# Performance work log

Measured on AMD Instinct MI355X. Metric: run time of the kernel, lower is better.

Reference implementation:

```python
import jax, jax.numpy as jnp
import numpy as np

N = 100_000      # nodes
E = 3_200_000    # directed edges (avg degree 32)
F_IN = 5         # node_features
H = 64           # hidden_dim


def setup_inputs() -> dict:
    key = jax.random.key(0)
    ks = jax.random.split(key, 11)
    x = jax.random.uniform(ks[0], (N, F_IN), dtype=jnp.float32)
    edge_index = jax.random.randint(ks[1], (2, E), 0, N, dtype=jnp.int32)
    def lin(k, fi, fo):
        kw, kb = jax.random.split(k)
        s = 1.0 / np.sqrt(fi)
        return (jax.random.uniform(kw, (fi, fo), jnp.float32, -s, s),
                jax.random.uniform(kb, (fo,), jnp.float32, -s, s))
    conv1_w, conv1_b = lin(ks[2], F_IN, H)
    conv2_w, conv2_b = lin(ks[3], H, H)
    lin1_w, lin1_b = lin(ks[4], H + 6, 32)
    lin2_w, lin2_b = lin(ks[5], 32, 2)
    return {"x": x, "edge_index": edge_index,
            "conv1_w": conv1_w, "conv1_b": conv1_b,
            "conv2_w": conv2_w, "conv2_b": conv2_b,
            "lin1_w": lin1_w, "lin1_b": lin1_b,
            "lin2_w": lin2_w, "lin2_b": lin2_b}


def _gcn_conv(x, src, dst, norm, W, b):
    # PyG GCNConv: out[dst] += norm_e * (x @ W)[src], then + bias
    h = x @ W                                   # [N, out]
    msg = h[src] * norm[:, None]                # [E+N, out] (gather, memory-bound)
    out = jax.ops.segment_sum(msg, dst, num_segments=N)
    return out + b


def _global_features(x):
    n_comp = jnp.sum(x[:, 2])
    n_and = jnp.sum(x[:, 3])
    n_or = jnp.sum(x[:, 4])
    comp_mask = (x[:, 2] == 1.0).astype(x.dtype)
    cnt = jnp.sum(comp_mask)
    safe = jnp.maximum(cnt, 1.0)
    avg_lambda = jnp.where(cnt > 0, jnp.sum(x[:, 0] * comp_mask) / safe, 0.0)
    avg_mu = jnp.where(cnt > 0, jnp.sum(x[:, 1] * comp_mask) / safe, 0.0)
    depth = n_and + n_or
    gf = jnp.stack([n_comp, n_and, n_or, depth, avg_lambda, avg_mu])[None, :]
    # original uses .item() -> constants, so no grad flows through these
    return jax.lax.stop_gradient(gf)


def reference(x, edge_index, conv1_w, conv1_b, conv2_w, conv2_b,
              lin1_w, lin1_b, lin2_w, lin2_b):
    loop = jnp.arange(N, dtype=edge_index.dtype)
    src = jnp.concatenate([edge_index[0], loop])   # add self-loops
    dst = jnp.concatenate([edge_index[1], loop])
    deg = jax.ops.segment_sum(jnp.ones_like(src, dtype=x.dtype), dst, num_segments=N)
    dinv = jnp.where(deg > 0, 1.0 / jnp.sqrt(deg), 0.0)
    norm = dinv[src] * dinv[dst]                   # [E+N]

    h = jax.nn.relu(_gcn_conv(x, src, dst, norm, conv1_w, conv1_b))
    h = jax.nn.relu(_gcn_conv(h, src, dst, norm, conv2_w, conv2_b))

    # global_mean_pool with batch == zeros -> mean over all nodes, one graph
    emb = jnp.mean(h, axis=0, keepdims=True)       # [1, H]
    emb = jnp.concatenate([emb, _global_features(x)], axis=1)  # [1, H+6]

    hid = jax.nn.relu(emb @ lin1_w + lin1_b)
    raw = hid @ lin2_w + lin2_b                    # [1, 2]
    return 2.0 + jax.nn.sigmoid(raw) * 3.0
```

## Files before the change

### kernel.cpp

```cpp
#include <hip/hip_runtime.h>
#include <hip/hip_bf16.h>
#include <math.h>


#define BUCKET 256
#define MAXB   512
#define NCHV   2048
#define Q      8
#define RCOPY  32

__global__ void k_hist(const int* __restrict__ dst, int E, int chunk,
                       int* __restrict__ gcounts, int NBK) {
    __shared__ int lcnt[MAXB];
    for (int i = threadIdx.x; i < NBK; i += blockDim.x) lcnt[i] = 0;
    __syncthreads();
    int e0 = blockIdx.x * chunk;
    int e1 = min(e0 + chunk, E);
    for (int e = e0 + threadIdx.x; e < e1; e += blockDim.x)
        atomicAdd(&lcnt[dst[e] >> 8], 1);
    __syncthreads();
    for (int b = threadIdx.x; b < NBK; b += blockDim.x)
        gcounts[blockIdx.x * NBK + b] = lcnt[b];
}

__global__ void k_colsum(const int* __restrict__ gcounts, int* __restrict__ btot,
                         int NBK, int NCH) {
    __shared__ int lds[256];
    int b = blockIdx.x, t = threadIdx.x;
    int s = 0;
    for (int c = t; c < NCH; c += 256) s += gcounts[c * NBK + b];
    lds[t] = s;
    __syncthreads();
    for (int off = 128; off; off >>= 1) {
        if (t < off) lds[t] += lds[t + off];
        __syncthreads();
    }
    if (t == 0) btot[b] = lds[0];
}

__global__ void k_scanA(const int* __restrict__ btot, int* __restrict__ bucket_base,
                        float* __restrict__ red, int NBK) {
    __shared__ int lds[MAXB];
    int t = threadIdx.x;
    for (int i = t; i < RCOPY * 64; i += MAXB) red[i] = 0.f;
    int v = (t < NBK) ? btot[t] : 0;
    lds[t] = v;
    __syncthreads();
    for (int off = 1; off < MAXB; off <<= 1) {
        int add = (t >= off) ? lds[t - off] : 0;
        __syncthreads();
        lds[t] += add;
        __syncthreads();
    }
    if (t < NBK) bucket_base[t] = lds[t] - v;
    if (t == NBK - 1) bucket_base[NBK] = lds[t];
}

__global__ void k_scanB(int* __restrict__ gcounts, const int* __restrict__ bucket_base,
                        int NBK, int NCH) {
    __shared__ int lds[512];
    int b = blockIdx.x, t = threadIdx.x;
    int carry = bucket_base[b];
    for (int base = 0; base < NCH; base += 512) {
        int c = base + t;
        int v = (c < NCH) ? gcounts[c * NBK + b] : 0;
        lds[t] = v;
        __syncthreads();
        for (int off = 1; off < 512; off <<= 1) {
            int add = (t >= off) ? lds[t - off] : 0;
            __syncthreads();
            lds[t] += add;
            __syncthreads();
        }
        if (c < NCH) gcounts[c * NBK + b] = carry + lds[t] - v;
        int tot = lds[511];
        __syncthreads();
        carry += tot;
    }
}

__global__ void k_bucketize(const int* __restrict__ src, const int* __restrict__ dst,
                            int E, int chunk, const int* __restrict__ gcounts,
                            int* __restrict__ records, int NBK) {
    __shared__ int lcur[MAXB];
    for (int b = threadIdx.x; b < NBK; b += blockDim.x)
        lcur[b] = gcounts[blockIdx.x * NBK + b];
    __syncthreads();
    int e0 = blockIdx.x * chunk;
    int e1 = min(e0 + chunk, E);
    for (int e = e0 + threadIdx.x; e < e1; e += blockDim.x) {
        int d = dst[e];
        int b = d >> 8;
        int rec = ((d & 255) << 17) | src[e];
        int slot = atomicAdd(&lcur[b], 1);
        records[slot] = rec;
    }
}

__global__ void k_csrA(const int* __restrict__ records, const int* __restrict__ bucket_base,
                       int* __restrict__ qhist) {
    __shared__ int cnt[BUCKET];
    int t = threadIdx.x, b = blockIdx.x, q = blockIdx.y;
    if (t < BUCKET) cnt[t] = 0;
    __syncthreads();
    int j0 = bucket_base[b], j1 = bucket_base[b + 1];
    int qlen = (j1 - j0 + Q - 1) / Q;
    int qs = j0 + q * qlen;
    int qe = min(qs + qlen, j1);
    for (int j = qs + t; j < qe; j += blockDim.x)
        atomicAdd(&cnt[records[j] >> 17], 1);
    __syncthreads();
    if (t < BUCKET) qhist[(b * Q + q) * BUCKET + t] = cnt[t];
}

__global__ void k_csrB(const int* __restrict__ qhist, const int* __restrict__ bucket_base,
                       const float* __restrict__ x,
                       int* __restrict__ qbase, int* __restrict__ pos,
                       int* __restrict__ rowend, float* __restrict__ dinv,
                       float* __restrict__ xs, float* __restrict__ gfpart, int n) {
    __shared__ int lds[BUCKET];
    __shared__ float gf6[8];
    int t = threadIdx.x, b = blockIdx.x;
    if (t < 8) gf6[t] = 0.f;
    int h[Q];
    int c = 0;
#pragma unroll
    for (int q = 0; q < Q; ++q) {
        h[q] = qhist[(b * Q + q) * BUCKET + t];
        c += h[q];
    }
    lds[t] = c;
    __syncthreads();
    for (int off = 1; off < BUCKET; off <<= 1) {
        int add = (t >= off) ? lds[t - off] : 0;
        __syncthreads();
        lds[t] += add;
        __syncthreads();
    }
    int j0 = bucket_base[b];
    int p = j0 + lds[t] - c;
    int run = p;
#pragma unroll
    for (int q = 0; q < Q; ++q) {
        qbase[(b * Q + q) * BUCKET + t] = run;
        run += h[q];
    }
    int node = b * BUCKET + t;
    float s2 = 0.f, s3 = 0.f, s4 = 0.f, sm0 = 0.f, sm1 = 0.f, sc = 0.f;
    if (node < n) {
        pos[node] = p;
        rowend[node] = p + c;
        float d = rsqrtf((float)(c + 1));
        dinv[node] = d;
        float x0 = x[node * 5 + 0], x1 = x[node * 5 + 1], x2 = x[node * 5 + 2];
        float x3 = x[node * 5 + 3], x4 = x[node * 5 + 4];
        float4 o;
        o.x = x0 * d; o.y = x1 * d; o.z = x2 * d; o.w = x3 * d;
        ((float4*)xs)[node * 2] = o;
        xs[node * 8 + 4] = x4 * d;
        s2 = x2; s3 = x3; s4 = x4;
        if (x2 == 1.0f) { sm0 = x0; sm1 = x1; sc = 1.f; }
    }
#pragma unroll
    for (int off = 32; off; off >>= 1) {
        s2 += __shfl_down(s2, off);
        s3 += __shfl_down(s3, off);
        s4 += __shfl_down(s4, off);
        sm0 += __shfl_down(sm0, off);
        sm1 += __shfl_down(sm1, off);
        sc += __shfl_down(sc, off);
    }
    if ((t & 63) == 0) {
        atomicAdd(&gf6[0], s2);
        atomicAdd(&gf6[1], s3);
        atomicAdd(&gf6[2], s4);
        atomicAdd(&gf6[3], sm0);
        atomicAdd(&gf6[4], sm1);
        atomicAdd(&gf6[5], sc);
    }
    __syncthreads();
    if (t < 6) gfpart[b * 8 + t] = gf6[t];
}

__global__ void k_csrC(const int* __restrict__ records, const int* __restrict__ bucket_base,
                       const int* __restrict__ qbase, int* __restrict__ ssrc) {
    __shared__ int cursor[BUCKET];
    int t = threadIdx.x, b = blockIdx.x, q = blockIdx.y;
    if (t < BUCKET) cursor[t] = qbase[(b * Q + q) * BUCKET + t];
    __syncthreads();
    int j0 = bucket_base[b], j1 = bucket_base[b + 1];
    int qlen = (j1 - j0 + Q - 1) / Q;
    int qs = j0 + q * qlen;
    int qe = min(qs + qlen, j1);
    for (int j = qs + t; j < qe; j += blockDim.x) {
        int rec = records[j];
        int slot = atomicAdd(&cursor[rec >> 17], 1);
        ssrc[slot] = rec & 131071;
    }
}

__global__ void k_agg5(const int* __restrict__ pos, const int* __restrict__ rowend,
                       const int* __restrict__ ssrc, const float* __restrict__ dinv,
                       const float* __restrict__ xs, float* __restrict__ agg5, int n) {
    int i = blockIdx.x * blockDim.x + threadIdx.x;
    if (i >= n) return;
    const float4* xs4 = (const float4*)xs;
    float4 a = xs4[i * 2];
    float a4 = xs[i * 8 + 4];
    int beg = pos[i], end = rowend[i];
    int j = beg;
    for (; j + 1 < end; j += 2) {
        int s0 = ssrc[j], s1 = ssrc[j + 1];
        float4 v0 = xs4[s0 * 2]; float w0 = xs[s0 * 8 + 4];
        float4 v1 = xs4[s1 * 2]; float w1 = xs[s1 * 8 + 4];
        a.x += v0.x + v1.x; a.y += v0.y + v1.y;
        a.z += v0.z + v1.z; a.w += v0.w + v1.w;
        a4 += w0 + w1;
    }
    for (; j < end; ++j) {
        int s = ssrc[j];
        float4 v = xs4[s * 2];
        a.x += v.x; a.y += v.y; a.z += v.z; a.w += v.w;
        a4 += xs[s * 8 + 4];
    }
    float dd = dinv[i];
    float4 o; o.x = a.x * dd; o.y = a.y * dd; o.z = a.z * dd; o.w = a.w * dd;
    ((float4*)agg5)[i * 2] = o;
    agg5[i * 8 + 4] = a4 * dd;
}

__global__ void k_h1(const float* __restrict__ agg5, const float* __restrict__ W1,
                     const float* __restrict__ b1, const float* __restrict__ dinv,
                     __hip_bfloat16* __restrict__ h1s, int n) {
    int t = blockIdx.x * blockDim.x + threadIdx.x;
    int i = t >> 6, f = t & 63;
    if (i >= n) return;
    float a0 = agg5[i * 8 + 0], a1 = agg5[i * 8 + 1], a2 = agg5[i * 8 + 2];
    float a3 = agg5[i * 8 + 3], a4 = agg5[i * 8 + 4];
    float v = a0 * W1[f] + a1 * W1[64 + f] + a2 * W1[128 + f]
            + a3 * W1[192 + f] + a4 * W1[256 + f] + b1[f];
    h1s[(size_t)i * 64 + f] = __float2bfloat16(dinv[i] * fmaxf(v, 0.f));
}

__global__ __launch_bounds__(256)
void k_l2fuse(const int* __restrict__ pos, const int* __restrict__ rowend,
              const int* __restrict__ ssrc, const float* __restrict__ dinv,
              const __hip_bfloat16* __restrict__ h1s, const float* __restrict__ W2,
              const float* __restrict__ b2, float* __restrict__ red, int n) {
    __shared__ float red64[64];
    int t = threadIdx.x, f = t & 63;
    if (t < 64) red64[t] = 0.f;
    __syncthreads();
    int w = blockIdx.x * (blockDim.x >> 6) + (t >> 6);
    int nw = gridDim.x * (blockDim.x >> 6);
    float bf = b2[f];
    float psum = 0.f;
    int nt = (n + 3) >> 2;
    for (int task = w; task < nt; task += nw) {
        int i0 = task * 4, i1 = i0 + 1, i2 = i0 + 2, i3 = i0 + 3;
        bool v1 = i1 < n, v2 = i2 < n, v3 = i3 < n;
        int p0 = pos[i0],            e0 = rowend[i0];
        int p1 = v1 ? pos[i1] : 0,   e1 = v1 ? rowend[i1] : 0;
        int p2 = v2 ? pos[i2] : 0,   e2 = v2 ? rowend[i2] : 0;
        int p3 = v3 ? pos[i3] : 0,   e3 = v3 ? rowend[i3] : 0;
        float a0 = __bfloat162float(h1s[(size_t)i0 * 64 + f]);
        float a1 = v1 ? __bfloat162float(h1s[(size_t)i1 * 64 + f]) : 0.f;
        float a2 = v2 ? __bfloat162float(h1s[(size_t)i2 * 64 + f]) : 0.f;
        float a3 = v3 ? __bfloat162float(h1s[(size_t)i3 * 64 + f]) : 0.f;
        int len = max(max(e0 - p0, e1 - p1), max(e2 - p2, e3 - p3));
#pragma unroll 2
        for (int m = 0; m < len; ++m) {
            int j0 = p0 + m, j1 = p1 + m, j2 = p2 + m, j3 = p3 + m;
            int s0 = ssrc[j0 < e0 ? j0 : 0];
            int s1 = ssrc[j1 < e1 ? j1 : 0];
            int s2 = ssrc[j2 < e2 ? j2 : 0];
            int s3 = ssrc[j3 < e3 ? j3 : 0];
            float g0 = __bfloat162float(h1s[(size_t)s0 * 64 + f]);
            float g1 = __bfloat162float(h1s[(size_t)s1 * 64 + f]);
            float g2 = __bfloat162float(h1s[(size_t)s2 * 64 + f]);
            float g3 = __bfloat162float(h1s[(size_t)s3 * 64 + f]);
            if (j0 < e0) a0 += g0;
            if (j1 < e1) a1 += g1;
            if (j2 < e2) a2 += g2;
            if (j3 < e3) a3 += g3;
        }
        float q0 = 0.f, q1 = 0.f, q2 = 0.f, q3 = 0.f;
#pragma unroll 8
        for (int k = 0; k < 64; ++k) {
            float w2v = W2[k * 64 + f];
            q0 += __shfl(a0, k) * w2v;
            q1 += __shfl(a1, k) * w2v;
            q2 += __shfl(a2, k) * w2v;
            q3 += __shfl(a3, k) * w2v;
        }
        psum += fmaxf(q0 * dinv[i0] + bf, 0.f);
        if (v1) psum += fmaxf(q1 * dinv[i1] + bf, 0.f);
        if (v2) psum += fmaxf(q2 * dinv[i2] + bf, 0.f);
        if (v3) psum += fmaxf(q3 * dinv[i3] + bf, 0.f);
    }
    atomicAdd(&red64[f], psum);
    __syncthreads();
    if (t < 64) atomicAdd(&red[(blockIdx.x & (RCOPY - 1)) * 64 + t], red64[t]);
}

__global__ void k_head(const float* __restrict__ red, const float* __restrict__ gfpart,
                       const float* __restrict__ l1w, const float* __restrict__ l1b,
                       const float* __restrict__ l2w, const float* __restrict__ l2b,
                       float* __restrict__ out, int n, int NBK) {
    __shared__ float emb[70];
    __shared__ float hid[32];
    int t = threadIdx.x;
    if (t < 64) {
        float s = 0.f;
#pragma unroll
        for (int c = 0; c < RCOPY; ++c) s += red[c * 64 + t];
        emb[t] = s / (float)n;
    }
    float g0 = 0.f, g1 = 0.f, g2 = 0.f, g3 = 0.f, g4 = 0.f, g5 = 0.f;
    for (int b = t; b < NBK; b += 64) {
        g0 += gfpart[b * 8 + 0]; g1 += gfpart[b * 8 + 1];
        g2 += gfpart[b * 8 + 2]; g3 += gfpart[b * 8 + 3];
        g4 += gfpart[b * 8 + 4]; g5 += gfpart[b * 8 + 5];
    }
#pragma unroll
    for (int off = 32; off; off >>= 1) {
        g0 += __shfl_down(g0, off); g1 += __shfl_down(g1, off);
        g2 += __shfl_down(g2, off); g3 += __shfl_down(g3, off);
        g4 += __shfl_down(g4, off); g5 += __shfl_down(g5, off);
    }
    if (t == 0) {
        float cnt = g5;
        float safe = fmaxf(cnt, 1.f);
        emb[64] = g0;
        emb[65] = g1;
        emb[66] = g2;
        emb[67] = g1 + g2;
        emb[68] = cnt > 0.f ? g3 / safe : 0.f;
        emb[69] = cnt > 0.f ? g4 / safe : 0.f;
    }
    __syncthreads();
    if (t < 32) {
        float acc = l1b[t];
#pragma unroll
        for (int k = 0; k < 70; ++k) acc += emb[k] * l1w[k * 32 + t];
        hid[t] = fmaxf(acc, 0.f);
    }
    __syncthreads();
    if (t < 2) {
        float acc = l2b[t];
#pragma unroll
        for (int j = 0; j < 32; ++j) acc += hid[j] * l2w[j * 2 + t];
        out[t] = 2.0f + 3.0f / (1.0f + expf(-acc));
    }
}

extern "C" void kernel_launch(void* const* d_in, const int* in_sizes, int n_in,
                              void* d_out, int out_size, void* d_ws, size_t ws_size,
                              hipStream_t stream) {
    const float* x   = (const float*)d_in[0];
    const int*   ei  = (const int*)d_in[1];
    const float* w1  = (const float*)d_in[2];
    const float* b1  = (const float*)d_in[3];
    const float* w2  = (const float*)d_in[4];
    const float* b2  = (const float*)d_in[5];
    const float* l1w = (const float*)d_in[6];
    const float* l1b = (const float*)d_in[7];
    const float* l2w = (const float*)d_in[8];
    const float* l2b = (const float*)d_in[9];

    const int n = in_sizes[0] / 5;
    const int E = in_sizes[1] / 2;
    const int* src = ei;
    const int* dst = ei + E;

    const int NBK = (n + BUCKET - 1) / BUCKET;
    const int NCH = NCHV;
    const int chunk = (E + NCH - 1) / NCH;

    size_t nf = (size_t)n * 64;
    __hip_bfloat16* h1s = (__hip_bfloat16*)d_ws;
    float* xs          = (float*)(h1s + nf);
    float* agg5        = xs + (size_t)n * 8;
    float* dinv        = agg5 + (size_t)n * 8;
    float* red         = dinv + n;
    float* gfpart      = red + RCOPY * 64;
    int*   pos         = (int*)(gfpart + (MAXB * 8));
    int*   rowend      = pos + n;
    int*   btot        = rowend + n;
    int*   bucket_base = btot + MAXB;
    int*   qhist       = bucket_base + (MAXB + 8);
    int*   qbase       = qhist + NBK * Q * BUCKET;
    int*   gcounts     = qbase + NBK * Q * BUCKET;
    int*   records     = gcounts + NCH * NBK;
    int*   ssrc        = records + E;

    k_hist<<<NCH, 512, 0, stream>>>(dst, E, chunk, gcounts, NBK);
    k_colsum<<<NBK, 256, 0, stream>>>(gcounts, btot, NBK, NCH);
    k_scanA<<<1, MAXB, 0, stream>>>(btot, bucket_base, red, NBK);
    k_scanB<<<NBK, 512, 0, stream>>>(gcounts, bucket_base, NBK, NCH);
    k_bucketize<<<NCH, 512, 0, stream>>>(src, dst, E, chunk, gcounts, records, NBK);

    dim3 qgrid(NBK, Q);
    k_csrA<<<qgrid, 512, 0, stream>>>(records, bucket_base, qhist);
    k_csrB<<<NBK, BUCKET, 0, stream>>>(qhist, bucket_base, x, qbase, pos, rowend,
                                       dinv, xs, gfpart, n);
    k_csrC<<<qgrid, 512, 0, stream>>>(records, bucket_base, qbase, ssrc);

    k_agg5<<<(n + 255) / 256, 256, 0, stream>>>(pos, rowend, ssrc, dinv, xs, agg5, n);
    k_h1<<<(int)((nf + 255) / 256), 256, 0, stream>>>(agg5, w1, b1, dinv, h1s, n);
    k_l2fuse<<<4096, 256, 0, stream>>>(pos, rowend, ssrc, dinv, h1s, w2, b2, red, n);

    k_head<<<1, 64, 0, stream>>>(red, gfpart, l1w, l1b, l2w, l2b, (float*)d_out, n, NBK);
}
```

Measured before the change: 265.0 us.

## Sort nodes by degree for balanced gathers; cache W2 in registers, 8 nodes/wave

```diff
diff --git a/kernel.cpp b/kernel.cpp
--- a/kernel.cpp
+++ b/kernel.cpp
@@ -8,6 +8,7 @@
 #define NCHV   2048
 #define Q      8
 #define RCOPY  32
+#define DNB    256
 
 __global__ void k_hist(const int* __restrict__ dst, int E, int chunk,
                        int* __restrict__ gcounts, int NBK) {
@@ -117,7 +118,8 @@
                        const float* __restrict__ x,
                        int* __restrict__ qbase, int* __restrict__ pos,
                        int* __restrict__ rowend, float* __restrict__ dinv,
-                       float* __restrict__ xs, float* __restrict__ gfpart, int n) {
+                       float* __restrict__ xs, float* __restrict__ gfpart,
+                       unsigned char* __restrict__ degb, int n) {
     __shared__ int lds[BUCKET];
     __shared__ float gf6[8];
     int t = threadIdx.x, b = blockIdx.x;
@@ -150,6 +152,7 @@
     if (node < n) {
         pos[node] = p;
         rowend[node] = p + c;
+        degb[node] = (unsigned char)(c < 255 ? c : 255);
         float d = rsqrtf((float)(c + 1));
         dinv[node] = d;
         float x0 = x[node * 5 + 0], x1 = x[node * 5 + 1], x2 = x[node * 5 + 2];
@@ -199,11 +202,63 @@
     }
 }
 
-__global__ void k_agg5(const int* __restrict__ pos, const int* __restrict__ rowend,
+__global__ void k_dhist(const unsigned char* __restrict__ degb, int n,
+                        int* __restrict__ dpart) {
+    __shared__ int bins[256];
+    int t = threadIdx.x, b = blockIdx.x;
+    bins[t] = 0;
+    __syncthreads();
+    int chunk = (n + DNB - 1) / DNB;
+    int i0 = b * chunk, i1 = min(i0 + chunk, n);
+    for (int i = i0 + t; i < i1; i += 256)
+        atomicAdd(&bins[degb[i]], 1);
+    __syncthreads();
+    dpart[b * 256 + t] = bins[t];
+}
+
+__global__ void k_dscan(int* __restrict__ dpart) {
+    __shared__ int lds[256];
+    int t = threadIdx.x;
+    int tot = 0;
+    for (int b = 0; b < DNB; ++b) tot += dpart[b * 256 + t];
+    lds[t] = tot;
+    __syncthreads();
+    for (int off = 1; off < 256; off <<= 1) {
+        int add = (t >= off) ? lds[t - off] : 0;
+        __syncthreads();
+        lds[t] += add;
+        __syncthreads();
+    }
+    int run = lds[t] - tot;
+    for (int b = 0; b < DNB; ++b) {
+        int v = dpart[b * 256 + t];
+        dpart[b * 256 + t] = run;
+        run += v;
+    }
+}
+
+__global__ void k_dscatter(const unsigned char* __restrict__ degb,
+                           const int* __restrict__ dpart, int n,
+                           int* __restrict__ perm) {
+    __shared__ int cur[256];
+    int t = threadIdx.x, b = blockIdx.x;
+    cur[t] = dpart[b * 256 + t];
+    __syncthreads();
+    int chunk = (n + DNB - 1) / DNB;
+    int i0 = b * chunk, i1 = min(i0 + chunk, n);
+    for (int i = i0 + t; i < i1; i += 256) {
+        int slot = atomicAdd(&cur[degb[i]], 1);
+        perm[slot] = i;
+    }
+}
+
+__global__ void k_agg5(const int* __restrict__ perm,
+                       const int* __restrict__ pos, const int* __restrict__ rowend,
                        const int* __restrict__ ssrc, const float* __restrict__ dinv,
                        const float* __restrict__ xs, float* __restrict__ agg5, int n) {
-    int i = blockIdx.x * blockDim.x + threadIdx.x;
-    if (i >= n) return;
+    int gid = blockIdx.x * blockDim.x + threadIdx.x;
+    if (gid >= n) return;
+    int i = perm[gid];
     const float4* xs4 = (const float4*)xs;
     float4 a = xs4[i * 2];
     float a4 = xs[i * 8 + 4];
@@ -243,7 +298,8 @@
 }
 
 __global__ __launch_bounds__(256)
-void k_l2fuse(const int* __restrict__ pos, const int* __restrict__ rowend,
+void k_l2fuse(const int* __restrict__ perm,
+              const int* __restrict__ pos, const int* __restrict__ rowend,
               const int* __restrict__ ssrc, const float* __restrict__ dinv,
               const __hip_bfloat16* __restrict__ h1s, const float* __restrict__ W2,
               const float* __restrict__ b2, float* __restrict__ red, int n) {
@@ -251,52 +307,46 @@
     int t = threadIdx.x, f = t & 63;
     if (t < 64) red64[t] = 0.f;
     __syncthreads();
+    float w2r[64];
+#pragma unroll
+    for (int k = 0; k < 64; ++k) w2r[k] = W2[k * 64 + f];
+    float bf = b2[f];
     int w = blockIdx.x * (blockDim.x >> 6) + (t >> 6);
     int nw = gridDim.x * (blockDim.x >> 6);
-    float bf = b2[f];
     float psum = 0.f;
-    int nt = (n + 3) >> 2;
+    int nt = (n + 7) >> 3;
     for (int task = w; task < nt; task += nw) {
-        int i0 = task * 4, i1 = i0 + 1, i2 = i0 + 2, i3 = i0 + 3;
-        bool v1 = i1 < n, v2 = i2 < n, v3 = i3 < n;
-        int p0 = pos[i0],            e0 = rowend[i0];
-        int p1 = v1 ? pos[i1] : 0,   e1 = v1 ? rowend[i1] : 0;
-        int p2 = v2 ? pos[i2] : 0,   e2 = v2 ? rowend[i2] : 0;
-        int p3 = v3 ? pos[i3] : 0,   e3 = v3 ? rowend[i3] : 0;
-        float a0 = __bfloat162float(h1s[(size_t)i0 * 64 + f]);
-        float a1 = v1 ? __bfloat162float(h1s[(size_t)i1 * 64 + f]) : 0.f;
-        float a2 = v2 ? __bfloat162float(h1s[(size_t)i2 * 64 + f]) : 0.f;
-        float a3 = v3 ? __bfloat162float(h1s[(size_t)i3 * 64 + f]) : 0.f;
-        int len = max(max(e0 - p0, e1 - p1), max(e2 - p2, e3 - p3));
+        int base = task * 8;
+#define SI(q) \
+        int i##q = (base + q < n) ? perm[base + q] : -1; \
+        bool v##q = i##q >= 0; \
+        int p##q = v##q ? pos[i##q] : 0; \
+        int e##q = v##q ? rowend[i##q] : 0; \
+        float a##q = v##q ? __bfloat162float(h1s[(size_t)i##q * 64 + f]) : 0.f;
+        SI(0) SI(1) SI(2) SI(3) SI(4) SI(5) SI(6) SI(7)
+#undef SI
+        int len = max(max(max(e0 - p0, e1 - p1), max(e2 - p2, e3 - p3)),
+                      max(max(e4 - p4, e5 - p5), max(e6 - p6, e7 - p7)));
 #pragma unroll 2
         for (int m = 0; m < len; ++m) {
-            int j0 = p0 + m, j1 = p1 + m, j2 = p2 + m, j3 = p3 + m;
-            int s0 = ssrc[j0 < e0 ? j0 : 0];
-            int s1 = ssrc[j1 < e1 ? j1 : 0];
-            int s2 = ssrc[j2 < e2 ? j2 : 0];
-            int s3 = ssrc[j3 < e3 ? j3 : 0];
-            float g0 = __bfloat162float(h1s[(size_t)s0 * 64 + f]);
-            float g1 = __bfloat162float(h1s[(size_t)s1 * 64 + f]);
-            float g2 = __bfloat162float(h1s[(size_t)s2 * 64 + f]);
-            float g3 = __bfloat162float(h1s[(size_t)s3 * 64 + f]);
-            if (j0 < e0) a0 += g0;
-            if (j1 < e1) a1 += g1;
-            if (j2 < e2) a2 += g2;
-            if (j3 < e3) a3 += g3;
+#define SS(q) \
+            { int j = p##q + m; \
+              int s = ssrc[j < e##q ? j : 0]; \
+              float g = __bfloat162float(h1s[(size_t)s * 64 + f]); \
+              if (j < e##q) a##q += g; }
+            SS(0) SS(1) SS(2) SS(3) SS(4) SS(5) SS(6) SS(7)
+#undef SS
         }
-        float q0 = 0.f, q1 = 0.f, q2 = 0.f, q3 = 0.f;
-#pragma unroll 8
-        for (int k = 0; k < 64; ++k) {
-            float w2v = W2[k * 64 + f];
-            q0 += __shfl(a0, k) * w2v;
-            q1 += __shfl(a1, k) * w2v;
-            q2 += __shfl(a2, k) * w2v;
-            q3 += __shfl(a3, k) * w2v;
-        }
-        psum += fmaxf(q0 * dinv[i0] + bf, 0.f);
-        if (v1) psum += fmaxf(q1 * dinv[i1] + bf, 0.f);
-        if (v2) psum += fmaxf(q2 * dinv[i2] + bf, 0.f);
-        if (v3) psum += fmaxf(q3 * dinv[i3] + bf, 0.f);
+#define SMM(q) { \
+        float qa = 0.f, qb = 0.f; \
+        _Pragma("unroll") \
+        for (int k = 0; k < 64; k += 2) { \
+            qa += __shfl(a##q, k) * w2r[k]; \
+            qb += __shfl(a##q, k + 1) * w2r[k + 1]; \
+        } \
+        if (v##q) psum += fmaxf((qa + qb) * dinv[i##q] + bf, 0.f); }
+        SMM(0) SMM(1) SMM(2) SMM(3) SMM(4) SMM(5) SMM(6) SMM(7)
+#undef SMM
     }
     atomicAdd(&red64[f], psum);
     __syncthreads();
@@ -390,7 +440,10 @@
     int*   bucket_base = btot + MAXB;
     int*   qhist       = bucket_base + (MAXB + 8);
     int*   qbase       = qhist + NBK * Q * BUCKET;
-    int*   gcounts     = qbase + NBK * Q * BUCKET;
+    int*   perm        = qbase + NBK * Q * BUCKET;
+    int*   dpart       = perm + n;
+    unsigned char* degb = (unsigned char*)(dpart + DNB * 256);
+    int*   gcounts     = (int*)(degb + ((n + 15) & ~15));
     int*   records     = gcounts + NCH * NBK;
     int*   ssrc        = records + E;
 
@@ -403,12 +456,20 @@
     dim3 qgrid(NBK, Q);
     k_csrA<<<qgrid, 512, 0, stream>>>(records, bucket_base, qhist);
     k_csrB<<<NBK, BUCKET, 0, stream>>>(qhist, bucket_base, x, qbase, pos, rowend,
-                                       dinv, xs, gfpart, n);
+                                       dinv, xs, gfpart, degb, n);
     k_csrC<<<qgrid, 512, 0, stream>>>(records, bucket_base, qbase, ssrc);
 
-    k_agg5<<<(n + 255) / 256, 256, 0, stream>>>(pos, rowend, ssrc, dinv, xs, agg5, n);
+    k_dhist<<<DNB, 256, 0, stream>>>(degb, n, dpart);
+    k_dscan<<<1, 256, 0, stream>>>(dpart);
+    k_dscatter<<<DNB, 256, 0, stream>>>(degb, dpart, n, perm);
+
+    k_agg5<<<(n + 255) / 256, 256, 0, stream>>>(perm, pos, rowend, ssrc, dinv, xs, agg5, n);
     k_h1<<<(int)((nf + 255) / 256), 256, 0, stream>>>(agg5, w1, b1, dinv, h1s, n);
-    k_l2fuse<<<4096, 256, 0, stream>>>(pos, rowend, ssrc, dinv, h1s, w2, b2, red, n);
+
+    const int nt = (n + 7) >> 3;
+    const int l2blocks = (nt + 3) / 4;
+    k_l2fuse<<<l2blocks, 256, 0, stream>>>(perm, pos, rowend, ssrc, dinv, h1s,
+                                           w2, b2, red, n);
 
     k_head<<<1, 64, 0, stream>>>(red, gfpart, l1w, l1b, l2w, l2b, (float*)d_out, n, NBK);
 }
```

After: 379.9 us. 1.43x slower.

## Split wavefront into two half-waves, each gathering packed bf16 pairs per node

Applied to the files above, without the earlier changes.

```diff
diff --git a/kernel.cpp b/kernel.cpp
--- a/kernel.cpp
+++ b/kernel.cpp
@@ -242,63 +242,75 @@
     h1s[(size_t)i * 64 + f] = __float2bfloat16(dinv[i] * fmaxf(v, 0.f));
 }
 
+__device__ __forceinline__ float bflo(unsigned int u) {
+    return __uint_as_float(u << 16);
+}
+__device__ __forceinline__ float bfhi(unsigned int u) {
+    return __uint_as_float(u & 0xFFFF0000u);
+}
+
 __global__ __launch_bounds__(256)
 void k_l2fuse(const int* __restrict__ pos, const int* __restrict__ rowend,
               const int* __restrict__ ssrc, const float* __restrict__ dinv,
               const __hip_bfloat16* __restrict__ h1s, const float* __restrict__ W2,
               const float* __restrict__ b2, float* __restrict__ red, int n) {
     __shared__ float red64[64];
-    int t = threadIdx.x, f = t & 63;
+    int t = threadIdx.x;
+    int lane = t & 63;
+    int half32 = lane & 32;
+    int fl = lane & 31;
+    int f0 = fl * 2;
     if (t < 64) red64[t] = 0.f;
     __syncthreads();
+    const unsigned int* h1u = (const unsigned int*)h1s;
+    float b2a = b2[f0], b2b = b2[f0 + 1];
     int w = blockIdx.x * (blockDim.x >> 6) + (t >> 6);
     int nw = gridDim.x * (blockDim.x >> 6);
-    float bf = b2[f];
-    float psum = 0.f;
-    int nt = (n + 3) >> 2;
+    float psum0 = 0.f, psum1 = 0.f;
+    int nt = (n + 1) >> 1;
     for (int task = w; task < nt; task += nw) {
-        int i0 = task * 4, i1 = i0 + 1, i2 = i0 + 2, i3 = i0 + 3;
-        bool v1 = i1 < n, v2 = i2 < n, v3 = i3 < n;
-        int p0 = pos[i0],            e0 = rowend[i0];
-        int p1 = v1 ? pos[i1] : 0,   e1 = v1 ? rowend[i1] : 0;
-        int p2 = v2 ? pos[i2] : 0,   e2 = v2 ? rowend[i2] : 0;
-        int p3 = v3 ? pos[i3] : 0,   e3 = v3 ? rowend[i3] : 0;
-        float a0 = __bfloat162float(h1s[(size_t)i0 * 64 + f]);
-        float a1 = v1 ? __bfloat162float(h1s[(size_t)i1 * 64 + f]) : 0.f;
-        float a2 = v2 ? __bfloat162float(h1s[(size_t)i2 * 64 + f]) : 0.f;
-        float a3 = v3 ? __bfloat162float(h1s[(size_t)i3 * 64 + f]) : 0.f;
-        int len = max(max(e0 - p0, e1 - p1), max(e2 - p2, e3 - p3));
-#pragma unroll 2
-        for (int m = 0; m < len; ++m) {
-            int j0 = p0 + m, j1 = p1 + m, j2 = p2 + m, j3 = p3 + m;
-            int s0 = ssrc[j0 < e0 ? j0 : 0];
-            int s1 = ssrc[j1 < e1 ? j1 : 0];
-            int s2 = ssrc[j2 < e2 ? j2 : 0];
-            int s3 = ssrc[j3 < e3 ? j3 : 0];
-            float g0 = __bfloat162float(h1s[(size_t)s0 * 64 + f]);
-            float g1 = __bfloat162float(h1s[(size_t)s1 * 64 + f]);
-            float g2 = __bfloat162float(h1s[(size_t)s2 * 64 + f]);
-            float g3 = __bfloat162float(h1s[(size_t)s3 * 64 + f]);
-            if (j0 < e0) a0 += g0;
-            if (j1 < e1) a1 += g1;
-            if (j2 < e2) a2 += g2;
-            if (j3 < e3) a3 += g3;
+        int i = task * 2 + (half32 >> 5);
+        bool vi = i < n;
+        int ci = vi ? i : 0;
+        int p = vi ? pos[ci] : 0;
+        int e = vi ? rowend[ci] : 0;
+        unsigned int u = h1u[(size_t)ci * 32 + fl];
+        float a0 = vi ? bflo(u) : 0.f;
+        float a1 = vi ? bfhi(u) : 0.f;
+        int j = p;
+        for (; j + 3 < e; j += 4) {
+            int s0 = ssrc[j], s1 = ssrc[j + 1], s2 = ssrc[j + 2], s3 = ssrc[j + 3];
+            unsigned int u0 = h1u[(size_t)s0 * 32 + fl];
+            unsigned int u1 = h1u[(size_t)s1 * 32 + fl];
+            unsigned int u2 = h1u[(size_t)s2 * 32 + fl];
+            unsigned int u3 = h1u[(size_t)s3 * 32 + fl];
+            a0 += (bflo(u0) + bflo(u1)) + (bflo(u2) + bflo(u3));
+            a1 += (bfhi(u0) + bfhi(u1)) + (bfhi(u2) + bfhi(u3));
         }
-        float q0 = 0.f, q1 = 0.f, q2 = 0.f, q3 = 0.f;
+        for (; j < e; ++j) {
+            unsigned int uu = h1u[(size_t)ssrc[j] * 32 + fl];
+            a0 += bflo(uu);
+            a1 += bfhi(uu);
+        }
+        float q0 = 0.f, q1 = 0.f;
 #pragma unroll 8
-        for (int k = 0; k < 64; ++k) {
-            float w2v = W2[k * 64 + f];
-            q0 += __shfl(a0, k) * w2v;
-            q1 += __shfl(a1, k) * w2v;
-            q2 += __shfl(a2, k) * w2v;
-            q3 += __shfl(a3, k) * w2v;
+        for (int q = 0; q < 32; ++q) {
+            int srcl = q + half32;
+            float a2q  = __shfl(a0, srcl);
+            float a2q1 = __shfl(a1, srcl);
+            float2 wa = *(const float2*)&W2[(2 * q) * 64 + f0];
+            float2 wb = *(const float2*)&W2[(2 * q + 1) * 64 + f0];
+            q0 += a2q * wa.x + a2q1 * wb.x;
+            q1 += a2q * wa.y + a2q1 * wb.y;
         }
-        psum += fmaxf(q0 * dinv[i0] + bf, 0.f);
-        if (v1) psum += fmaxf(q1 * dinv[i1] + bf, 0.f);
-        if (v2) psum += fmaxf(q2 * dinv[i2] + bf, 0.f);
-        if (v3) psum += fmaxf(q3 * dinv[i3] + bf, 0.f);
-    }
-    atomicAdd(&red64[f], psum);
+        if (vi) {
+            float dd = dinv[i];
+            psum0 += fmaxf(q0 * dd + b2a, 0.f);
+            psum1 += fmaxf(q1 * dd + b2b, 0.f);
+        }
+    }
+    atomicAdd(&red64[f0], psum0);
+    atomicAdd(&red64[f0 + 1], psum1);
     __syncthreads();
     if (t < 64) atomicAdd(&red[(blockIdx.x & (RCOPY - 1)) * 64 + t], red64[t]);
 }
@@ -408,6 +420,7 @@
 
     k_agg5<<<(n + 255) / 256, 256, 0, stream>>>(pos, rowend, ssrc, dinv, xs, agg5, n);
     k_h1<<<(int)((nf + 255) / 256), 256, 0, stream>>>(agg5, w1, b1, dinv, h1s, n);
+
     k_l2fuse<<<4096, 256, 0, stream>>>(pos, rowend, ssrc, dinv, h1s, w2, b2, red, n);
 
     k_head<<<1, 64, 0, stream>>>(red, gfpart, l1w, l1b, l2w, l2b, (float*)d_out, n, NBK);
```

New measurement: 314.7 us. 1.19x slower.
